# Performance work log

Measured on AMD Instinct MI355X. Metric: run time of the kernel, lower is better.

Reference implementation:

```python
import jax, jax.numpy as jnp
import numpy as np

D = 1024
EPS = 1e-5

def layer_norm(x, g, b):
    m = jnp.mean(x, axis=-1, keepdims=True)
    v = jnp.mean(jnp.square(x - m), axis=-1, keepdims=True)
    return (x - m) * jax.lax.rsqrt(v + EPS) * g + b

def setup_inputs() -> dict:
    key = jax.random.key(0)
    ks = jax.random.split(key, 8)
    S, B = 4096, 4
    s = 1.0 / np.sqrt(D)
    return {
        "x": jax.random.normal(ks[0], (S, B, D), dtype=jnp.float32),
        "W_v": jax.random.uniform(ks[1], (D, D), jnp.float32, -s, s),
        "theta": jax.random.uniform(ks[2], (D, D), jnp.float32, -s, s),
        "ln1_g": jnp.ones((D,), jnp.float32),
        "ln1_b": jnp.zeros((D,), jnp.float32),
        "ln2_g": jnp.ones((D,), jnp.float32),
        "ln2_b": jnp.zeros((D,), jnp.float32),
        "w1": jax.random.uniform(ks[3], (4 * D, D), jnp.float32, -s, s),
        "b1": jnp.zeros((4 * D,), jnp.float32),
        "w2": jax.random.uniform(ks[4], (D, 4 * D), jnp.float32, -1.0 / np.sqrt(4 * D), 1.0 / np.sqrt(4 * D)),
        "b2": jnp.zeros((D,), jnp.float32),
    }

def reference(x, W_v, theta, ln1_g, ln1_b, ln2_g, ln2_b, w1, b1, w2, b2):
    # x: [S, B, D]
    h = layer_norm(x, ln1_g, ln1_b)
    X = jnp.transpose(h, (1, 0, 2))          # [B, n, D], n = S
    n = X.shape[1]
    XWv = X @ W_v.T                          # [B, n, D]
    Xth = X @ theta.T                        # [B, n, D]
    # first term: (1/n) * ones(n,n) @ XWv == seq-mean broadcast over rows
    first = jnp.mean(XWv, axis=1, keepdims=True)
    # second term reassociated: (X @ theta(X)^T) @ XWv == X @ (theta(X)^T @ XWv)
    M = jnp.einsum('bnd,bne->bde', Xth, XWv)  # [B, D, D]
    second = (1.0 / (n * np.sqrt(D))) * jnp.einsum('bnd,bde->bne', X, M)
    attn = first + second                    # [B, n, D]
    X = X + attn
    h = jnp.transpose(X, (1, 0, 2))          # [S, B, D]
    h2 = layer_norm(h, ln2_g, ln2_b)
    mlp = jax.nn.gelu(h2 @ w1.T + b1, approximate=False) @ w2.T + b2
    return h + mlp
```

## Files before the change

### kernel.cpp

```cpp
#include <hip/hip_runtime.h>
#include <math.h>

#define S_ 4096
#define B_ 4
#define D_ 1024
#define R_ (S_*B_)
#define H_ (4*D_)

typedef unsigned short u16;
typedef unsigned int   u32;
typedef __attribute__((ext_vector_type(8))) short bf16x8;
typedef __attribute__((ext_vector_type(4))) float f32x4;

__device__ __forceinline__ u16 f2bf(float f) {
  u32 u = __float_as_uint(f);
  u32 r = (u + 0x7fffu + ((u >> 16) & 1u)) >> 16;
  return (u16)r;
}
__device__ __forceinline__ float bf2f(u16 u) {
  return __uint_as_float(((u32)u) << 16);
}

__device__ __forceinline__ void gl_lds16(const u16* g, u16* l) {
  __builtin_amdgcn_global_load_lds((const __attribute__((address_space(1))) void*)g,
                                   (__attribute__((address_space(3))) void*)l,
                                   16, 0, 0);
}
__device__ __forceinline__ void BAR() {
  asm volatile("s_barrier" ::: "memory");
}
#define VM(N) asm volatile("s_waitcnt vmcnt(" #N ")" ::: "memory")

__device__ __forceinline__ float gelu_f(float t) {
  const float u2 = 1.5957691216f * t + 0.0713548162726f * t * t * t;
  return t / (1.0f + __expf(-u2));
}

__device__ __forceinline__ void mfma16(const bf16x8* af, const bf16x8* bfr, f32x4* a) {
  __builtin_amdgcn_s_setprio(1);
  #pragma unroll
  for (int mi = 0; mi < 4; ++mi)
    #pragma unroll
    for (int ni = 0; ni < 4; ++ni)
      a[mi*4+ni] = __builtin_amdgcn_mfma_f32_16x16x32_bf16(af[mi], bfr[ni], a[mi*4+ni], 0, 0, 0);
  __builtin_amdgcn_s_setprio(0);
}

__global__ __launch_bounds__(256) void f2bf_k(const float* __restrict__ in,
                                              u16* __restrict__ out, int n4) {
  int i = blockIdx.x * 256 + threadIdx.x;
  if (i < n4) {
    float4 v = ((const float4*)in)[i];
    ushort4 o = make_ushort4(f2bf(v.x), f2bf(v.y), f2bf(v.z), f2bf(v.w));
    ((ushort4*)out)[i] = o;
  }
}

template<bool TR>
__global__ __launch_bounds__(256) void ln_k(const float* __restrict__ x,
                                            u16* __restrict__ o,
                                            const float* __restrict__ g,
                                            const float* __restrict__ bb) {
  const int row = blockIdx.x;
  const int tid = threadIdx.x;
  const float4 v = *(const float4*)&x[(long)row * D_ + tid * 4];
  float vv[4] = {v.x, v.y, v.z, v.w};
  float s = vv[0] + vv[1] + vv[2] + vv[3];
  float q = vv[0]*vv[0] + vv[1]*vv[1] + vv[2]*vv[2] + vv[3]*vv[3];
  const int l = tid & 63, w = tid >> 6;
  #pragma unroll
  for (int off = 32; off > 0; off >>= 1) {
    s += __shfl_down(s, off, 64);
    q += __shfl_down(q, off, 64);
  }
  __shared__ float red[8];
  if (l == 0) { red[w] = s; red[4 + w] = q; }
  __syncthreads();
  s = red[0] + red[1] + red[2] + red[3];
  q = red[4] + red[5] + red[6] + red[7];
  const float m   = s * (1.0f / D_);
  const float var = q * (1.0f / D_) - m * m;
  const float inv = rsqrtf(var + 1e-5f);
  const long orow = TR ? ((long)(row % B_) * S_ + (row / B_)) : (long)row;
  const int j = tid * 4;
  ushort4 ou = make_ushort4(
      f2bf((vv[0] - m) * inv * g[j+0] + bb[j+0]),
      f2bf((vv[1] - m) * inv * g[j+1] + bb[j+1]),
      f2bf((vv[2] - m) * inv * g[j+2] + bb[j+2]),
      f2bf((vv[3] - m) * inv * g[j+3] + bb[j+3]));
  *(ushort4*)&o[orow * D_ + j] = ou;
}

template<int EPI>
__global__ __launch_bounds__(256, 2) void gemm_k(
    const u16* __restrict__ A, long sAz,
    const u16* __restrict__ B, long sBz,
    int K, int ldc,
    u16* __restrict__ Cb, long sCz,
    float* __restrict__ Cf,
    const float* __restrict__ vec1,
    float scale)
{
  const int bz = blockIdx.z;
  const u16* Ab = A + (long)bz * sAz;
  const u16* Bb = B + (long)bz * sBz;
  const int row0 = blockIdx.x * 128;
  const int col0 = blockIdx.y * 128;
  const int lda = K;

  __shared__ __align__(16) u16 As[128 * 32];
  __shared__ __align__(16) u16 Bs[128 * 32];

  const int tid = threadIdx.x;
  const int w = tid >> 6;
  const int l = tid & 63;
  const int wr = (w >> 1) * 64;
  const int wc = (w & 1) * 64;

  f32x4 acc[4][4];
  #pragma unroll
  for (int mi = 0; mi < 4; ++mi)
    #pragma unroll
    for (int ni = 0; ni < 4; ++ni) acc[mi][ni] = (f32x4){0.f, 0.f, 0.f, 0.f};

  const int lrow = l & 15;
  const int lo   = l >> 4;

  for (int k0 = 0; k0 < K; k0 += 32) {
    __syncthreads();
    #pragma unroll
    for (int it = 0; it < 2; ++it) {
      const int cb = it * 256 + (w << 6);
      const int c  = cb + l;
      const int r  = c >> 2;
      const int qs = ((c & 3) ^ ((r >> 1) & 3)) << 3;
      gl_lds16(Ab + (long)(row0 + r) * lda + (k0 + qs), &As[cb << 3]);
      gl_lds16(Bb + (long)(col0 + r) * lda + (k0 + qs), &Bs[cb << 3]);
    }
    __syncthreads();

    bf16x8 af[4], bfr[4];
    #pragma unroll
    for (int mi = 0; mi < 4; ++mi) {
      const int R = wr + mi * 16 + lrow;
      af[mi]  = *(const bf16x8*)&As[R * 32 + ((lo ^ ((R >> 1) & 3)) << 3)];
    }
    #pragma unroll
    for (int ni = 0; ni < 4; ++ni) {
      const int R = wc + ni * 16 + lrow;
      bfr[ni] = *(const bf16x8*)&Bs[R * 32 + ((lo ^ ((R >> 1) & 3)) << 3)];
    }
    #pragma unroll
    for (int mi = 0; mi < 4; ++mi)
      #pragma unroll
      for (int ni = 0; ni < 4; ++ni)
        acc[mi][ni] = __builtin_amdgcn_mfma_f32_16x16x32_bf16(af[mi], bfr[ni], acc[mi][ni], 0, 0, 0);
  }

  const int rbase = row0 + wr + (lo << 2);
  const int cbase = col0 + wc + lrow;
  #pragma unroll
  for (int mi = 0; mi < 4; ++mi)
    #pragma unroll
    for (int ni = 0; ni < 4; ++ni)
      #pragma unroll
      for (int r = 0; r < 4; ++r) {
        const int i = rbase + mi * 16 + r;
        const int j = cbase + ni * 16;
        if constexpr (EPI == 0)
          Cb[(long)bz * sCz + (long)i * ldc + j] = f2bf(acc[mi][ni][r]);
      }
  (void)Cf; (void)vec1; (void)scale;
}

#define ACC(A_, NI_) acc[(((A_) >> 2) << 4) + (((A_) & 3) << 2) + (NI_)]

#define RD_B(CUR, KH) \
  bfr[0] = *(const bf16x8*)(pB + (CUR)*16384 + (KH)*8192 + 0);    \
  bfr[1] = *(const bf16x8*)(pB + (CUR)*16384 + (KH)*8192 + 512);  \
  bfr[2] = *(const bf16x8*)(pB + (CUR)*16384 + (KH)*8192 + 1024); \
  bfr[3] = *(const bf16x8*)(pB + (CUR)*16384 + (KH)*8192 + 1536);

#define RD_A(CUR, KH, MH) \
  af[0] = *(const bf16x8*)(pA + (CUR)*16384 + (KH)*8192 + (MH)*2048 + 0);    \
  af[1] = *(const bf16x8*)(pA + (CUR)*16384 + (KH)*8192 + (MH)*2048 + 512);  \
  af[2] = *(const bf16x8*)(pA + (CUR)*16384 + (KH)*8192 + (MH)*2048 + 1024); \
  af[3] = *(const bf16x8*)(pA + (CUR)*16384 + (KH)*8192 + (MH)*2048 + 1536);

#define STG(OP, KREL) \
  if (4 * kt2 + (KREL) < NKH) { \
    const u16* s_ = (OP ? pGB : pGA) + (KREL) * 32; \
    u16* d_ = LdsFu + (OP)*32768 + ((((KREL) >> 1) & 1))*16384 + (((KREL) & 1))*8192 + wst; \
    gl_lds16(s_, d_); \
    gl_lds16(s_ + gK16, d_ + 512); \
  }

#define ITER(CUR) { \
    const int kt = 2 * kt2 + (CUR); \
    RD_B(CUR, 0) RD_A(CUR, 0, 0) \
    STG(0, 3 + 2*(CUR)) \
    BAR(); \
    mfma16(af, bfr, acc); \
    BAR(); \
    RD_A(CUR, 0, 1) \
    STG(1, 3 + 2*(CUR)) \
    if (kt == NT - 1) { VM(0); } else { VM(8); } \
    BAR(); \
    mfma16(af, bfr, acc + 16); \
    BAR(); \
    RD_B(CUR, 1) RD_A(CUR, 1, 0) \
    STG(0, 4 + 2*(CUR)) \
    BAR(); \
    mfma16(af, bfr, acc); \
    BAR(); \
    RD_A(CUR, 1, 1) \
    STG(1, 4 + 2*(CUR)) \
    if (kt < NT - 2) { VM(8); } else if (kt == NT - 2) { VM(4); } else { VM(0); } \
    BAR(); \
    mfma16(af, bfr, acc + 16); \
    BAR(); \
  }

template<int EPI>
__global__ __launch_bounds__(512, 1) void gemm256_k(
    const u16* __restrict__ A, long sAz,
    const u16* __restrict__ B, long sBz,
    int K, int ldc,
    u16* __restrict__ Cb, long sCz,
    float* __restrict__ Cf,
    const float* __restrict__ vec1,
    float scale)
{
  const int bz = blockIdx.z;
  const u16* Ab = A + (long)bz * sAz;
  const u16* Bb = B + (long)bz * sBz;
  const int row0 = blockIdx.x * 256;
  const int col0 = blockIdx.y * 256;

  __shared__ __align__(16) u16 LdsFu[8 * 256 * 32];

  const int tid = threadIdx.x;
  const int w   = tid >> 6;
  const int l   = tid & 63;
  const int wm  = w >> 2;
  const int wn  = w & 3;
  const int lr  = l & 15;
  const int lo  = l >> 4;

  const int NKH = K >> 5;
  const int NT  = K >> 6;

  const int rs   = w * 32 + (l >> 2);
  const int qsrc = ((l & 3) ^ ((l >> 3) & 3)) << 3;
  const int qsw  = (lo ^ ((lr >> 1) & 3)) << 3;
  const int wst  = w * 1024;
  const long gK16 = (long)16 * K;

  const u16* pA = LdsFu + (wm * 128 + lr) * 32 + qsw;
  const u16* pB = LdsFu + 32768 + (wn * 64 + lr) * 32 + qsw;
  const u16* pGA = Ab + (long)(row0 + rs) * K + qsrc;
  const u16* pGB = Bb + (long)(col0 + rs) * K + qsrc;

  f32x4 acc[32];
  #pragma unroll
  for (int i = 0; i < 32; ++i) acc[i] = (f32x4){0.f, 0.f, 0.f, 0.f};

  {
    auto PSTG = [&](int khg, int op) {
      if (khg >= NKH) return;
      const u16* s = (op ? pGB : pGA) + khg * 32;
      u16* d = LdsFu + op * 32768 + ((khg >> 1) & 1) * 16384 + (khg & 1) * 8192 + wst;
      gl_lds16(s, d);
      gl_lds16(s + gK16, d + 512);
    };
    PSTG(0, 0); PSTG(0, 1);
    PSTG(1, 0); PSTG(1, 1);
    PSTG(2, 0); PSTG(2, 1);
  }
  VM(8);
  BAR();

  {
    bf16x8 af[4], bfr[4];
    const int NT2 = NT >> 1;
    for (int kt2 = 0; kt2 < NT2; ++kt2) {
      ITER(0)
      ITER(1)
      pGA += 128;
      pGB += 128;
    }
  }

  if constexpr (EPI == 4) {
    const int b = row0 / S_;
    if (bz == 0) {
      #pragma unroll
      for (int ni = 0; ni < 4; ++ni) {
        float s = 0.f;
        #pragma unroll
        for (int a = 0; a < 8; ++a)
          #pragma unroll
          for (int r = 0; r < 4; ++r) s += ACC(a, ni)[r];
        s += __shfl_down(s, 16, 64);
        s += __shfl_down(s, 32, 64);
        if (lo == 0) atomicAdd(&Cf[b * D_ + (col0 + wn * 64 + ni * 16 + lr)], s);
      }
    }
    u16* Tw = LdsFu + w * (64 * 68);
    u16* dst = Cb + (long)bz * sCz + (long)b * D_ * S_;
    const long ib0 = (row0 % S_) + wm * 128;
    #pragma unroll
    for (int p = 0; p < 2; ++p) {
      #pragma unroll
      for (int mi = 0; mi < 4; ++mi) {
        const int a = p * 4 + mi;
        #pragma unroll
        for (int ni = 0; ni < 4; ++ni) {
          ushort4 pk = make_ushort4(f2bf(ACC(a, ni)[0]), f2bf(ACC(a, ni)[1]),
                                    f2bf(ACC(a, ni)[2]), f2bf(ACC(a, ni)[3]));
          *(ushort4*)&Tw[(ni * 16 + lr) * 68 + mi * 16 + lo * 4] = pk;
        }
      }
      #pragma unroll
      for (int it = 0; it < 8; ++it) {
        const int jj = it * 8 + (l >> 3);
        const int ic = (l & 7) * 8;
        bf16x8 v = *(const bf16x8*)&Tw[jj * 68 + ic];
        *(bf16x8*)&dst[(long)(col0 + wn * 64 + jj) * S_ + (ib0 + p * 64 + ic)] = v;
      }
    }
  } else {
    float* E = (float*)LdsFu;
    const int wbase = w * (32 * 72);
    #pragma unroll
    for (int p = 0; p < 4; ++p) {
      #pragma unroll
      for (int mh = 0; mh < 2; ++mh) {
        const int a = ((p >> 1) << 2) + ((p & 1) << 1) + mh;
        #pragma unroll
        for (int ni = 0; ni < 4; ++ni)
          #pragma unroll
          for (int r = 0; r < 4; ++r)
            E[wbase + (mh * 16 + lo * 4 + r) * 72 + ni * 16 + lr] = ACC(a, ni)[r];
      }
      #pragma unroll
      for (int rr = 0; rr < 8; ++rr) {
        const int rl = (l >> 4) + rr * 4;
        const int cl = (l & 15) * 4;
        const f32x4 v = *(const f32x4*)&E[wbase + rl * 72 + cl];
        const long i = row0 + wm * 128 + p * 32 + rl;
        const int  j = col0 + wn * 64 + cl;
        if constexpr (EPI == 0) {
          ushort4 o = make_ushort4(f2bf(v[0]), f2bf(v[1]), f2bf(v[2]), f2bf(v[3]));
          *(ushort4*)&Cb[(long)bz * sCz + i * ldc + j] = o;
        } else if constexpr (EPI == 1) {
          const ushort4 xv = *(const ushort4*)&Ab[i * K + j];
          const f32x4 f1 = *(const f32x4*)&vec1[bz * D_ + j];
          f32x4 o;
          o[0] = bf2f(xv.x) + f1[0] * (1.0f / S_) + scale * v[0];
          o[1] = bf2f(xv.y) + f1[1] * (1.0f / S_) + scale * v[1];
          o[2] = bf2f(xv.z) + f1[2] * (1.0f / S_) + scale * v[2];
          o[3] = bf2f(xv.w) + f1[3] * (1.0f / S_) + scale * v[3];
          *(f32x4*)&Cf[(i * B_ + bz) * (long)D_ + j] = o;
        } else if constexpr (EPI == 2) {
          const f32x4 b = *(const f32x4*)&vec1[j];
          ushort4 o = make_ushort4(f2bf(gelu_f(v[0] + b[0])),
                                   f2bf(gelu_f(v[1] + b[1])),
                                   f2bf(gelu_f(v[2] + b[2])),
                                   f2bf(gelu_f(v[3] + b[3])));
          *(ushort4*)&Cb[i * ldc + j] = o;
        } else {
          const f32x4 b = *(const f32x4*)&vec1[j];
          f32x4 c = *(const f32x4*)&Cf[i * ldc + j];
          c[0] += v[0] + b[0]; c[1] += v[1] + b[1];
          c[2] += v[2] + b[2]; c[3] += v[3] + b[3];
          *(f32x4*)&Cf[i * ldc + j] = c;
        }
      }
    }
  }
}

extern "C" void kernel_launch(void* const* d_in, const int* in_sizes, int n_in,
                              void* d_out, int out_size, void* d_ws, size_t ws_size,
                              hipStream_t stream) {
  (void)in_sizes; (void)n_in; (void)out_size; (void)ws_size;
  const float* x     = (const float*)d_in[0];
  const float* W_v   = (const float*)d_in[1];
  const float* theta = (const float*)d_in[2];
  const float* ln1g  = (const float*)d_in[3];
  const float* ln1b  = (const float*)d_in[4];
  const float* ln2g  = (const float*)d_in[5];
  const float* ln2b  = (const float*)d_in[6];
  const float* w1    = (const float*)d_in[7];
  const float* b1    = (const float*)d_in[8];
  const float* w2    = (const float*)d_in[9];
  const float* b2    = (const float*)d_in[10];
  float* out = (float*)d_out;

  char* ws = (char*)d_ws;
  const size_t MB = 1024ull * 1024ull;
  u16*   Wv_bf = (u16*)(ws + 0);
  u16*   Th_bf = (u16*)(ws + 2 * MB);
  u16*   w1_bf = (u16*)(ws + 4 * MB);
  u16*   w2_bf = (u16*)(ws + 12 * MB);
  float* first = (float*)(ws + 20 * MB);
  u16*   Mt    = (u16*)(ws + 21 * MB);
  u16*   Xn    = (u16*)(ws + 29 * MB);
  u16*   XWvT  = (u16*)(ws + 61 * MB);
  u16*   XthT  = (u16*)(ws + 93 * MB);
  u16*   h2    = (u16*)(ws + 29 * MB);
  u16*   G     = (u16*)(ws + 61 * MB);

  f2bf_k<<<dim3((D_*D_/4 + 255)/256), 256, 0, stream>>>(W_v,   Wv_bf, D_*D_/4);
  f2bf_k<<<dim3((D_*D_/4 + 255)/256), 256, 0, stream>>>(theta, Th_bf, D_*D_/4);
  f2bf_k<<<dim3((H_*D_/4 + 255)/256), 256, 0, stream>>>(w1,    w1_bf, H_*D_/4);
  f2bf_k<<<dim3((H_*D_/4 + 255)/256), 256, 0, stream>>>(w2,    w2_bf, H_*D_/4);

  ln_k<true><<<dim3(R_), 256, 0, stream>>>(x, Xn, ln1g, ln1b);

  hipMemsetAsync(first, 0, B_ * D_ * sizeof(float), stream);
  gemm256_k<4><<<dim3(R_/256, D_/256, 2), 512, 0, stream>>>(
      Xn, 0, Wv_bf, (long)D_*D_, D_, D_,
      XWvT, (long)D_*S_*B_, first, nullptr, 0.f);

  gemm_k<0><<<dim3(D_/128, D_/128, B_), 256, 0, stream>>>(
      XWvT, (long)D_*S_, XthT, (long)D_*S_, S_, D_, Mt, (long)D_*D_, nullptr, nullptr, 0.f);

  gemm256_k<1><<<dim3(S_/256, D_/256, B_), 512, 0, stream>>>(
      Xn, (long)S_*D_, Mt, (long)D_*D_, D_, D_, nullptr, 0, out, first,
      1.0f / ((float)S_ * 32.0f));

  ln_k<false><<<dim3(R_), 256, 0, stream>>>(out, h2, ln2g, ln2b);

  gemm256_k<2><<<dim3(R_/256, H_/256, 1), 512, 0, stream>>>(
      h2, 0, w1_bf, 0, D_, H_, G, 0, nullptr, b1, 0.f);
  gemm256_k<3><<<dim3(R_/256, D_/256, 1), 512, 0, stream>>>(
      G, 0, w2_bf, 0, H_, D_, nullptr, 0, out, b2, 0.f);
}
```

Measured before the change: 558.4 us.

## Replace 256x256 GEMM tile kernel with 128x128 tile kernel at higher occupancy

The 256x256-tile, 8-wave bf16 MFMA GEMM is replaced by a 128x128-tile kernel with 8 waves, each computing a 64x32 sub-tile and holding 8 accumulators instead of 32. Launch bounds now allow 4 blocks per CU, and the K-loop staging pipeline is reworked to a two-phase double buffer. The LDS-staged vectorised epilogues for the non-transposed outputs are replaced by direct scalar per-element stores. The aim is more occupancy and more blocks across CUs, traded against roughly double global/LDS traffic per FLOP and uncoalesced scalar epilogue writes.

```diff
diff --git a/kernel.cpp b/kernel.cpp
--- a/kernel.cpp
+++ b/kernel.cpp
@@ -36,13 +36,13 @@
   return t / (1.0f + __expf(-u2));
 }
 
-__device__ __forceinline__ void mfma16(const bf16x8* af, const bf16x8* bfr, f32x4* a) {
+__device__ __forceinline__ void mfma8(const bf16x8* af, const bf16x8* bfr, f32x4* a) {
   __builtin_amdgcn_s_setprio(1);
   #pragma unroll
   for (int mi = 0; mi < 4; ++mi)
     #pragma unroll
-    for (int ni = 0; ni < 4; ++ni)
-      a[mi*4+ni] = __builtin_amdgcn_mfma_f32_16x16x32_bf16(af[mi], bfr[ni], a[mi*4+ni], 0, 0, 0);
+    for (int ni = 0; ni < 2; ++ni)
+      a[mi*2+ni] = __builtin_amdgcn_mfma_f32_16x16x32_bf16(af[mi], bfr[ni], a[mi*2+ni], 0, 0, 0);
   __builtin_amdgcn_s_setprio(0);
 }
 
@@ -173,56 +173,41 @@
   (void)Cf; (void)vec1; (void)scale;
 }
 
-#define ACC(A_, NI_) acc[(((A_) >> 2) << 4) + (((A_) & 3) << 2) + (NI_)]
-
-#define RD_B(CUR, KH) \
-  bfr[0] = *(const bf16x8*)(pB + (CUR)*16384 + (KH)*8192 + 0);    \
-  bfr[1] = *(const bf16x8*)(pB + (CUR)*16384 + (KH)*8192 + 512);  \
-  bfr[2] = *(const bf16x8*)(pB + (CUR)*16384 + (KH)*8192 + 1024); \
-  bfr[3] = *(const bf16x8*)(pB + (CUR)*16384 + (KH)*8192 + 1536);
-
-#define RD_A(CUR, KH, MH) \
-  af[0] = *(const bf16x8*)(pA + (CUR)*16384 + (KH)*8192 + (MH)*2048 + 0);    \
-  af[1] = *(const bf16x8*)(pA + (CUR)*16384 + (KH)*8192 + (MH)*2048 + 512);  \
-  af[2] = *(const bf16x8*)(pA + (CUR)*16384 + (KH)*8192 + (MH)*2048 + 1024); \
-  af[3] = *(const bf16x8*)(pA + (CUR)*16384 + (KH)*8192 + (MH)*2048 + 1536);
-
-#define STG(OP, KREL) \
-  if (4 * kt2 + (KREL) < NKH) { \
-    const u16* s_ = (OP ? pGB : pGA) + (KREL) * 32; \
-    u16* d_ = LdsFu + (OP)*32768 + ((((KREL) >> 1) & 1))*16384 + (((KREL) & 1))*8192 + wst; \
-    gl_lds16(s_, d_); \
-    gl_lds16(s_ + gK16, d_ + 512); \
-  }
-
-#define ITER(CUR) { \
+
+#define RD128(CUR, KH) \
+  bfr[0] = *(const bf16x8*)(pB + (CUR)*8192 + (KH)*4096 + 0);    \
+  bfr[1] = *(const bf16x8*)(pB + (CUR)*8192 + (KH)*4096 + 512);  \
+  af[0]  = *(const bf16x8*)(pA + (CUR)*8192 + (KH)*4096 + 0);    \
+  af[1]  = *(const bf16x8*)(pA + (CUR)*8192 + (KH)*4096 + 512);  \
+  af[2]  = *(const bf16x8*)(pA + (CUR)*8192 + (KH)*4096 + 1024); \
+  af[3]  = *(const bf16x8*)(pA + (CUR)*8192 + (KH)*4096 + 1536);
+
+#define STG128(OP, KOFF, DB, KH) \
+  if (4 * kt2 + (KOFF) < NKH) { \
+    gl_lds16((OP ? pGB : pGA) + (KOFF) * 32, \
+             L + (OP)*16384 + (DB)*8192 + (KH)*4096 + (w << 9)); \
+  }
+
+#define ITER128(CUR) { \
     const int kt = 2 * kt2 + (CUR); \
-    RD_B(CUR, 0) RD_A(CUR, 0, 0) \
-    STG(0, 3 + 2*(CUR)) \
+    RD128(CUR, 0) \
+    STG128(0, 2*(CUR)+3, ((CUR)^1), 1) \
+    STG128(1, 2*(CUR)+3, ((CUR)^1), 1) \
+    if (kt >= NT - 2) { VM(0); } else { VM(4); } \
     BAR(); \
-    mfma16(af, bfr, acc); \
+    mfma8(af, bfr, acc); \
     BAR(); \
-    RD_A(CUR, 0, 1) \
-    STG(1, 3 + 2*(CUR)) \
-    if (kt == NT - 1) { VM(0); } else { VM(8); } \
+    RD128(CUR, 1) \
+    STG128(0, 2*(CUR)+4, (CUR), 0) \
+    STG128(1, 2*(CUR)+4, (CUR), 0) \
+    if (kt >= NT - 2) { VM(0); } else { VM(4); } \
     BAR(); \
-    mfma16(af, bfr, acc + 16); \
+    mfma8(af, bfr, acc); \
     BAR(); \
-    RD_B(CUR, 1) RD_A(CUR, 1, 0) \
-    STG(0, 4 + 2*(CUR)) \
-    BAR(); \
-    mfma16(af, bfr, acc); \
-    BAR(); \
-    RD_A(CUR, 1, 1) \
-    STG(1, 4 + 2*(CUR)) \
-    if (kt < NT - 2) { VM(8); } else if (kt == NT - 2) { VM(4); } else { VM(0); } \
-    BAR(); \
-    mfma16(af, bfr, acc + 16); \
-    BAR(); \
   }
 
 template<int EPI>
-__global__ __launch_bounds__(512, 1) void gemm256_k(
+__global__ __launch_bounds__(512, 4) void g128_k(
     const u16* __restrict__ A, long sAz,
     const u16* __restrict__ B, long sBz,
     int K, int ldc,
@@ -234,10 +219,10 @@
   const int bz = blockIdx.z;
   const u16* Ab = A + (long)bz * sAz;
   const u16* Bb = B + (long)bz * sBz;
-  const int row0 = blockIdx.x * 256;
-  const int col0 = blockIdx.y * 256;
-
-  __shared__ __align__(16) u16 LdsFu[8 * 256 * 32];
+  const int row0 = blockIdx.x * 128;
+  const int col0 = blockIdx.y * 128;
+
+  __shared__ __align__(16) u16 L[8 * 128 * 32];
 
   const int tid = threadIdx.x;
   const int w   = tid >> 6;
@@ -250,42 +235,38 @@
   const int NKH = K >> 5;
   const int NT  = K >> 6;
 
-  const int rs   = w * 32 + (l >> 2);
-  const int qsrc = ((l & 3) ^ ((l >> 3) & 3)) << 3;
+  const int rs   = w * 16 + (l >> 2);
+  const int qsrc = ((l & 3) ^ ((rs >> 1) & 3)) << 3;
   const int qsw  = (lo ^ ((lr >> 1) & 3)) << 3;
-  const int wst  = w * 1024;
-  const long gK16 = (long)16 * K;
-
-  const u16* pA = LdsFu + (wm * 128 + lr) * 32 + qsw;
-  const u16* pB = LdsFu + 32768 + (wn * 64 + lr) * 32 + qsw;
+
+  const u16* pA = L + (wm * 64 + lr) * 32 + qsw;
+  const u16* pB = L + 16384 + (wn * 32 + lr) * 32 + qsw;
   const u16* pGA = Ab + (long)(row0 + rs) * K + qsrc;
   const u16* pGB = Bb + (long)(col0 + rs) * K + qsrc;
 
-  f32x4 acc[32];
-  #pragma unroll
-  for (int i = 0; i < 32; ++i) acc[i] = (f32x4){0.f, 0.f, 0.f, 0.f};
+  f32x4 acc[8];
+  #pragma unroll
+  for (int i = 0; i < 8; ++i) acc[i] = (f32x4){0.f, 0.f, 0.f, 0.f};
 
   {
-    auto PSTG = [&](int khg, int op) {
-      if (khg >= NKH) return;
-      const u16* s = (op ? pGB : pGA) + khg * 32;
-      u16* d = LdsFu + op * 32768 + ((khg >> 1) & 1) * 16384 + (khg & 1) * 8192 + wst;
-      gl_lds16(s, d);
-      gl_lds16(s + gK16, d + 512);
-    };
-    PSTG(0, 0); PSTG(0, 1);
-    PSTG(1, 0); PSTG(1, 1);
-    PSTG(2, 0); PSTG(2, 1);
-  }
-  VM(8);
+    int kt2 = 0; (void)kt2;
+    #pragma unroll
+    for (int khg = 0; khg < 4; ++khg) {
+      if (khg < NKH) {
+        gl_lds16(pGA + khg * 32, L + ((khg >> 1) & 1) * 8192 + (khg & 1) * 4096 + (w << 9));
+        gl_lds16(pGB + khg * 32, L + 16384 + ((khg >> 1) & 1) * 8192 + (khg & 1) * 4096 + (w << 9));
+      }
+    }
+  }
+  VM(4);
   BAR();
 
   {
-    bf16x8 af[4], bfr[4];
+    bf16x8 af[4], bfr[2];
     const int NT2 = NT >> 1;
     for (int kt2 = 0; kt2 < NT2; ++kt2) {
-      ITER(0)
-      ITER(1)
+      ITER128(0)
+      ITER128(1)
       pGA += 128;
       pGB += 128;
     }
@@ -295,86 +276,57 @@
     const int b = row0 / S_;
     if (bz == 0) {
       #pragma unroll
-      for (int ni = 0; ni < 4; ++ni) {
+      for (int ni = 0; ni < 2; ++ni) {
         float s = 0.f;
         #pragma unroll
-        for (int a = 0; a < 8; ++a)
+        for (int mi = 0; mi < 4; ++mi)
           #pragma unroll
-          for (int r = 0; r < 4; ++r) s += ACC(a, ni)[r];
+          for (int r = 0; r < 4; ++r) s += acc[mi*2+ni][r];
         s += __shfl_down(s, 16, 64);
         s += __shfl_down(s, 32, 64);
-        if (lo == 0) atomicAdd(&Cf[b * D_ + (col0 + wn * 64 + ni * 16 + lr)], s);
-      }
-    }
-    u16* Tw = LdsFu + w * (64 * 68);
+        if (lo == 0) atomicAdd(&Cf[b * D_ + (col0 + wn * 32 + ni * 16 + lr)], s);
+      }
+    }
+    u16* Tw = L + w * (32 * 68);
     u16* dst = Cb + (long)bz * sCz + (long)b * D_ * S_;
-    const long ib0 = (row0 % S_) + wm * 128;
-    #pragma unroll
-    for (int p = 0; p < 2; ++p) {
-      #pragma unroll
-      for (int mi = 0; mi < 4; ++mi) {
-        const int a = p * 4 + mi;
+    const long ib0 = (row0 % S_) + wm * 64;
+    #pragma unroll
+    for (int mi = 0; mi < 4; ++mi)
+      #pragma unroll
+      for (int ni = 0; ni < 2; ++ni) {
+        ushort4 pk = make_ushort4(f2bf(acc[mi*2+ni][0]), f2bf(acc[mi*2+ni][1]),
+                                  f2bf(acc[mi*2+ni][2]), f2bf(acc[mi*2+ni][3]));
+        *(ushort4*)&Tw[(ni * 16 + lr) * 68 + mi * 16 + lo * 4] = pk;
+      }
+    #pragma unroll
+    for (int it = 0; it < 4; ++it) {
+      const int jj = it * 8 + (l >> 3);
+      const int ic = (l & 7) * 8;
+      bf16x8 v = *(const bf16x8*)&Tw[jj * 68 + ic];
+      *(bf16x8*)&dst[(long)(col0 + wn * 32 + jj) * S_ + (ib0 + ic)] = v;
+    }
+  } else {
+    #pragma unroll
+    for (int mi = 0; mi < 4; ++mi) {
+      #pragma unroll
+      for (int ni = 0; ni < 2; ++ni) {
         #pragma unroll
-        for (int ni = 0; ni < 4; ++ni) {
-          ushort4 pk = make_ushort4(f2bf(ACC(a, ni)[0]), f2bf(ACC(a, ni)[1]),
-                                    f2bf(ACC(a, ni)[2]), f2bf(ACC(a, ni)[3]));
-          *(ushort4*)&Tw[(ni * 16 + lr) * 68 + mi * 16 + lo * 4] = pk;
-        }
-      }
-      #pragma unroll
-      for (int it = 0; it < 8; ++it) {
-        const int jj = it * 8 + (l >> 3);
-        const int ic = (l & 7) * 8;
-        bf16x8 v = *(const bf16x8*)&Tw[jj * 68 + ic];
-        *(bf16x8*)&dst[(long)(col0 + wn * 64 + jj) * S_ + (ib0 + p * 64 + ic)] = v;
-      }
-    }
-  } else {
-    float* E = (float*)LdsFu;
-    const int wbase = w * (32 * 72);
-    #pragma unroll
-    for (int p = 0; p < 4; ++p) {
-      #pragma unroll
-      for (int mh = 0; mh < 2; ++mh) {
-        const int a = ((p >> 1) << 2) + ((p & 1) << 1) + mh;
-        #pragma unroll
-        for (int ni = 0; ni < 4; ++ni)
-          #pragma unroll
-          for (int r = 0; r < 4; ++r)
-            E[wbase + (mh * 16 + lo * 4 + r) * 72 + ni * 16 + lr] = ACC(a, ni)[r];
-      }
-      #pragma unroll
-      for (int rr = 0; rr < 8; ++rr) {
-        const int rl = (l >> 4) + rr * 4;
-        const int cl = (l & 15) * 4;
-        const f32x4 v = *(const f32x4*)&E[wbase + rl * 72 + cl];
-        const long i = row0 + wm * 128 + p * 32 + rl;
-        const int  j = col0 + wn * 64 + cl;
-        if constexpr (EPI == 0) {
-          ushort4 o = make_ushort4(f2bf(v[0]), f2bf(v[1]), f2bf(v[2]), f2bf(v[3]));
-          *(ushort4*)&Cb[(long)bz * sCz + i * ldc + j] = o;
-        } else if constexpr (EPI == 1) {
-          const ushort4 xv = *(const ushort4*)&Ab[i * K + j];
-          const f32x4 f1 = *(const f32x4*)&vec1[bz * D_ + j];
-          f32x4 o;
-          o[0] = bf2f(xv.x) + f1[0] * (1.0f / S_) + scale * v[0];
-          o[1] = bf2f(xv.y) + f1[1] * (1.0f / S_) + scale * v[1];
-          o[2] = bf2f(xv.z) + f1[2] * (1.0f / S_) + scale * v[2];
-          o[3] = bf2f(xv.w) + f1[3] * (1.0f / S_) + scale * v[3];
-          *(f32x4*)&Cf[(i * B_ + bz) * (long)D_ + j] = o;
-        } else if constexpr (EPI == 2) {
-          const f32x4 b = *(const f32x4*)&vec1[j];
-          ushort4 o = make_ushort4(f2bf(gelu_f(v[0] + b[0])),
-                                   f2bf(gelu_f(v[1] + b[1])),
-                                   f2bf(gelu_f(v[2] + b[2])),
-                                   f2bf(gelu_f(v[3] + b[3])));
-          *(ushort4*)&Cb[i * ldc + j] = o;
-        } else {
-          const f32x4 b = *(const f32x4*)&vec1[j];
-          f32x4 c = *(const f32x4*)&Cf[i * ldc + j];
-          c[0] += v[0] + b[0]; c[1] += v[1] + b[1];
-          c[2] += v[2] + b[2]; c[3] += v[3] + b[3];
-          *(f32x4*)&Cf[i * ldc + j] = c;
+        for (int r = 0; r < 4; ++r) {
+          const long i = row0 + wm * 64 + mi * 16 + lo * 4 + r;
+          const int  j = col0 + wn * 32 + ni * 16 + lr;
+          const float a = acc[mi*2+ni][r];
+          if constexpr (EPI == 0) {
+            Cb[(long)bz * sCz + i * ldc + j] = f2bf(a);
+          } else if constexpr (EPI == 1) {
+            const float xv = bf2f(Ab[i * K + j]);
+            Cf[(i * B_ + bz) * (long)D_ + j] =
+                xv + vec1[bz * D_ + j] * (1.0f / S_) + scale * a;
+          } else if constexpr (EPI == 2) {
+            Cb[i * ldc + j] = f2bf(gelu_f(a + vec1[j]));
+          } else {
+            const long idx = i * ldc + j;
+            Cf[idx] = Cf[idx] + a + vec1[j];
+          }
         }
       }
     }
@@ -420,21 +372,21 @@
   ln_k<true><<<dim3(R_), 256, 0, stream>>>(x, Xn, ln1g, ln1b);
 
   hipMemsetAsync(first, 0, B_ * D_ * sizeof(float), stream);
-  gemm256_k<4><<<dim3(R_/256, D_/256, 2), 512, 0, stream>>>(
+  g128_k<4><<<dim3(R_/128, D_/128, 2), 512, 0, stream>>>(
       Xn, 0, Wv_bf, (long)D_*D_, D_, D_,
       XWvT, (long)D_*S_*B_, first, nullptr, 0.f);
 
   gemm_k<0><<<dim3(D_/128, D_/128, B_), 256, 0, stream>>>(
       XWvT, (long)D_*S_, XthT, (long)D_*S_, S_, D_, Mt, (long)D_*D_, nullptr, nullptr, 0.f);
 
-  gemm256_k<1><<<dim3(S_/256, D_/256, B_), 512, 0, stream>>>(
+  g128_k<1><<<dim3(S_/128, D_/128, B_), 512, 0, stream>>>(
       Xn, (long)S_*D_, Mt, (long)D_*D_, D_, D_, nullptr, 0, out, first,
       1.0f / ((float)S_ * 32.0f));
 
   ln_k<false><<<dim3(R_), 256, 0, stream>>>(out, h2, ln2g, ln2b);
 
-  gemm256_k<2><<<dim3(R_/256, H_/256, 1), 512, 0, stream>>>(
+  g128_k<2><<<dim3(R_/128, H_/128, 1), 512, 0, stream>>>(
       h2, 0, w1_bf, 0, D_, H_, G, 0, nullptr, b1, 0.f);
-  gemm256_k<3><<<dim3(R_/256, D_/256, 1), 512, 0, stream>>>(
+  g128_k<3><<<dim3(R_/128, D_/128, 1), 512, 0, stream>>>(
       G, 0, w2_bf, 0, H_, D_, nullptr, 0, out, b2, 0.f);
 }
```

Result: slower. 633.3 us (+13.4%).
